# Optimization experiments

Measured on AMD Instinct MI355X. Metric: run time of the kernel, lower is better.

## Reference

```python
import jax, jax.numpy as jnp
import numpy as np

B, L, C, H, W = 4, 8, 32, 128, 256
M1, M2 = 32, 32  # spectral modes


def setup_inputs() -> dict:
    key = jax.random.key(0)
    k1, k2, k3, k4, k5, k6 = jax.random.split(key, 6)
    scale = 1.0 / (C * C)
    return {
        "x": jax.random.normal(k1, (B, L, C, H, W), dtype=jnp.float32),
        "k": jax.random.normal(k2, (C, H, W), dtype=jnp.float32),
        "w1r": scale * jax.random.normal(k3, (C, C, M1, M2), dtype=jnp.float32),
        "w1i": scale * jax.random.normal(k4, (C, C, M1, M2), dtype=jnp.float32),
        "w2r": scale * jax.random.normal(k5, (C, C, M1, M2), dtype=jnp.float32),
        "w2i": scale * jax.random.normal(k6, (C, C, M1, M2), dtype=jnp.float32),
    }


def reference(x, k, w1r, w1i, w2r, w2i):
    # x: [B, L, C, H, W] real; k: [C, H, W] conv kernel (broadcast over B*L).
    b, l, c, h, w = x.shape
    # --- FlashFFTConvInterface fallback path: circular conv via rfft2.
    # H, W are already 2/3/5-smooth (next_fast_len is identity -> no padding).
    u = x.reshape(b * l, c, h, w)
    u_f = jnp.fft.rfft2(u)                     # [B*L, C, H, W//2+1] complex
    k_f = jnp.fft.rfft2(k)                     # [C, H, W//2+1], broadcasts
    y = jnp.fft.irfft2(u_f * k_f, s=(h, w)).reshape(b, l, c, h, w)

    # --- SpectralConv2d: per-mode channel mixing in frequency domain.
    x_f = jnp.fft.rfft2(y)                     # [B, L, C, H, Wf] complex
    wf = x_f.shape[-1]
    w1 = (w1r + 1j * w1i).astype(x_f.dtype)
    w2 = (w2r + 1j * w2i).astype(x_f.dtype)
    m1 = min(h, M1)
    m2 = min(wf, M2)
    co = w1.shape[1]
    top = jnp.einsum('blcij,coij->bloij', x_f[:, :, :, :m1, :m2], w1[:, :, :m1, :m2])
    out_f = jnp.zeros((b, l, co, h, wf), dtype=x_f.dtype)
    out_f = out_f.at[:, :, :, :m1, :m2].set(top)
    if h > 1 and (h > M1 or wf > M2):
        bot = jnp.einsum('blcij,coij->bloij', x_f[:, :, :, h - m1:, :m2], w2[:, :, :m1, :m2])
        out_f = out_f.at[:, :, :, h - m1:, :m2].set(bot)
    return jnp.fft.irfft2(out_f, s=(h, w))    # [B, L, Co, H, W] real
```

## Files before the change

kernel.cpp:

```cpp
#include <hip/hip_runtime.h>
#include <math.h>

#define Hn 128
#define Wn 256
#define PLANE (Hn*Wn)

#define OFF_TQC 0u
#define OFF_TQS 2048u
#define OFF_TP  4096u
#define OFF_KM  16384u
#define OFF_XM  147456u
#define OFF_B   4341760u
#define OFF_RK  12730368u

__global__ __launch_bounds__(256) void build_tables(float* __restrict__ ws) {
  int tid = blockIdx.x * 256 + threadIdx.x;
  const double PI2 = 6.283185307179586476925286766559;
  if (tid < 512) {
    int j = tid >> 4, xi = tid & 15;
    float cc[4], ss[4];
#pragma unroll
    for (int m = 0; m < 4; m++) {
      int x = xi * 4 + m;
      double ang = PI2 * (double)((j * x) & 255) / 256.0;
      cc[m] = (float)cos(ang); ss[m] = (float)sin(ang);
    }
    ((float4*)(ws + OFF_TQC))[tid] = make_float4(cc[0], cc[1], cc[2], cc[3]);
    ((float4*)(ws + OFF_TQS))[tid] = make_float4(ss[0], ss[1], ss[2], ss[3]);
  }
  if (tid < 2048) {
    int p = tid >> 6, y2 = tid & 63;
    double a0 = PI2 * (double)((p * (2 * y2)) & 127) / 128.0;
    double a1 = PI2 * (double)((p * (2 * y2 + 1)) & 127) / 128.0;
    ((float4*)(ws + OFF_TP))[tid] =
        make_float4((float)cos(a0), (float)sin(a0), (float)cos(a1), (float)sin(a1));
  }
}

__global__ __launch_bounds__(256, 3) void fwd_rows(const float* __restrict__ src,
                                                   float2* __restrict__ R,
                                                   const float* __restrict__ ws) {
  int plane = blockIdx.x >> 2, chunk = blockIdx.x & 3;
  __shared__ __align__(16) float Sd[32 * 260];
  __shared__ float4 Tc[544], Ts[544];
  int t = threadIdx.x;
  const float4* src4 = (const float4*)src;
  size_t sb = (size_t)plane * 8192 + (size_t)chunk * 2048;
#pragma unroll
  for (int k = 0; k < 8; k++) {
    int idx = t + 256 * k;
    int row = idx >> 6, c4 = idx & 63;
    int sws = (row >> 1) & 15;
    *(float4*)&Sd[row * 260 + ((c4 ^ sws) << 2)] = src4[sb + idx];
  }
  const float4* gTc = (const float4*)(ws + OFF_TQC);
  const float4* gTs = (const float4*)(ws + OFF_TQS);
#pragma unroll
  for (int k = 0; k < 2; k++) {
    int idx = t + 256 * k;
    Tc[(idx >> 4) * 17 + (idx & 15)] = gTc[idx];
    Ts[(idx >> 4) * 17 + (idx & 15)] = gTs[idx];
  }
  __syncthreads();
  float eA[4][4], oA[4][4];
#pragma unroll
  for (int uu = 0; uu < 4; uu++) {
    int unit = uu * 256 + t;
    int y = unit >> 5, xb = unit & 31;
    int sws = (y >> 1) & 15;
    const float* rowp = &Sd[y * 260];
    float4 A = *(const float4*)&rowp[(xb ^ sws) << 2];
    float Av[4] = {A.x, A.y, A.z, A.w};
    float M[4];
#pragma unroll
    for (int kk = 0; kk < 4; kk++) {
      int xm = 256 - 4 * xb - kk;
      int xmc = (xm > 255) ? 255 : xm;
      int c4m = xmc >> 2, e = xmc & 3;
      float v = rowp[((c4m ^ sws) << 2) + e];
      M[kk] = (xm > 255) ? 0.f : v;
    }
#pragma unroll
    for (int kk = 0; kk < 4; kk++) {
      eA[uu][kk] = Av[kk] + M[kk];
      oA[uu][kk] = Av[kk] - M[kk];
    }
    if (xb == 0) {
      oA[uu][0] = rowp[(32 ^ sws) << 2];
    }
  }
  __syncthreads();
#pragma unroll
  for (int uu = 0; uu < 4; uu++) {
    int unit = uu * 256 + t;
    int y = unit >> 5, xb = unit & 31;
    int sws = (y >> 1) & 15;
    float* rowp = &Sd[y * 260];
    *(float4*)&rowp[(xb ^ sws) << 2] =
        make_float4(eA[uu][0], eA[uu][1], eA[uu][2], eA[uu][3]);
    *(float4*)&rowp[((32 + xb) ^ sws) << 2] =
        make_float4(oA[uu][0], oA[uu][1], oA[uu][2], oA[uu][3]);
  }
  __syncthreads();
  int jg = t & 15, yg = t >> 4;
  int jm = jg & 3;
  const float4* pC0 = &Tc[jg * 17];
  const float4* pS0 = &Ts[jg * 17];
  const float4* pC1 = &Tc[(jg + 16) * 17];
  const float4* pS1 = &Ts[(jg + 16) * 17];
  const float4* p2_0 = (jm & 1) ? pS0 : pC0;
  const float4* p4_0 = (jm & 1) ? pC0 : pS0;
  const float4* p2_1 = (jm & 1) ? pS1 : pC1;
  const float4* p4_1 = (jm & 1) ? pC1 : pS1;
  float sa = (jm == 0 || jm == 3) ? 1.f : -1.f;
  float sb_ = (jm < 2) ? 1.f : -1.f;
  float pm = (jg & 1) ? -1.f : 1.f;
  int sw = yg & 15;
  const float* row0 = &Sd[(2 * yg) * 260];
  const float* row1 = &Sd[(2 * yg + 1) * 260];
  float d1[2][2], d2[2][2], d3[2][2], d4[2][2];
#pragma unroll
  for (int a = 0; a < 2; a++)
#pragma unroll
    for (int b = 0; b < 2; b++) { d1[a][b] = 0.f; d2[a][b] = 0.f; d3[a][b] = 0.f; d4[a][b] = 0.f; }
#define DOT4(a, b) (a.x * b.x + a.y * b.y + a.z * b.z + a.w * b.w)
#pragma unroll 4
  for (int xb = 0; xb < 16; xb++) {
    int off = (xb ^ sw) << 2;
    float4 e0y0 = *(const float4*)&row0[off];
    float4 e1y0 = *(const float4*)&row0[off + 64];
    float4 o0y0 = *(const float4*)&row0[off + 128];
    float4 o1y0 = *(const float4*)&row0[off + 192];
    float4 e0y1 = *(const float4*)&row1[off];
    float4 e1y1 = *(const float4*)&row1[off + 64];
    float4 o0y1 = *(const float4*)&row1[off + 128];
    float4 o1y1 = *(const float4*)&row1[off + 192];
    float4 c0 = pC0[xb], s0 = pS0[xb];
    float4 t20 = p2_0[xb], t40 = p4_0[xb];
    float4 c1 = pC1[xb], s1 = pS1[xb];
    float4 t21 = p2_1[xb], t41 = p4_1[xb];
    d1[0][0] += DOT4(e0y0, c0);  d1[0][1] += DOT4(e0y1, c0);
    d1[1][0] += DOT4(e0y0, c1);  d1[1][1] += DOT4(e0y1, c1);
    d2[0][0] += DOT4(e1y0, t20); d2[0][1] += DOT4(e1y1, t20);
    d2[1][0] += DOT4(e1y0, t21); d2[1][1] += DOT4(e1y1, t21);
    d3[0][0] += DOT4(o0y0, s0);  d3[0][1] += DOT4(o0y1, s0);
    d3[1][0] += DOT4(o0y0, s1);  d3[1][1] += DOT4(o0y1, s1);
    d4[0][0] += DOT4(o1y0, t40); d4[0][1] += DOT4(o1y1, t40);
    d4[1][0] += DOT4(o1y0, t41); d4[1][1] += DOT4(o1y1, t41);
  }
#undef DOT4
  float u128_0 = row0[128 + 4 * sw];
  float u128_1 = row1[128 + 4 * sw];
#pragma unroll
  for (int jj = 0; jj < 2; jj++) {
    int j = jg + 16 * jj;
#pragma unroll
    for (int ky = 0; ky < 2; ky++) {
      int y = chunk * 32 + yg * 2 + ky;
      float u128 = ky ? u128_1 : u128_0;
      float re = d1[jj][ky] + sa * d2[jj][ky] + pm * u128;
      float im = -(d3[jj][ky] + sb_ * d4[jj][ky]);
      R[((size_t)plane * 128 + y) * 32 + j] = make_float2(re, im);
    }
  }
}

__global__ __launch_bounds__(256) void fwd_cols(const float2* __restrict__ Rg,
                                                float2* __restrict__ dst,
                                                const float* __restrict__ ws) {
  int plane = blockIdx.x;
  __shared__ float4 Rs4[2048];
  __shared__ float4 TPs[2048];
  float2* Rs = (float2*)Rs4;
  int t = threadIdx.x;
  const float4* in4 = (const float4*)(Rg + (size_t)plane * 4096);
#pragma unroll
  for (int k = 0; k < 8; k++) Rs4[t + 256 * k] = in4[t + 256 * k];
  const float4* gTP = (const float4*)(ws + OFF_TP);
#pragma unroll
  for (int k = 0; k < 8; k++) TPs[t + 256 * k] = gTP[t + 256 * k];
  __syncthreads();
  int j = t & 31, pg = t >> 5;
  float Are[4], Aim[4], Bre[4], Bim[4];
#pragma unroll
  for (int m = 0; m < 4; m++) { Are[m] = Aim[m] = Bre[m] = Bim[m] = 0.f; }
  for (int it = 0; it < 32; it++) {
#pragma unroll
    for (int h = 0; h < 2; h++) {
      int y2 = 2 * it + h;
      float sg = (h == 0) ? 1.f : -1.f;
      float2 r0 = Rs[(2 * y2) * 32 + j];
      float2 r1 = Rs[(2 * y2 + 1) * 32 + j];
#pragma unroll
      for (int m = 0; m < 4; m++) {
        int p = pg + 8 * m;
        float4 tw = TPs[p * 64 + y2];
        float P0 = r0.x * tw.x + r0.y * tw.y;
        float Q0 = r0.y * tw.x - r0.x * tw.y;
        float P1 = r1.x * tw.z + r1.y * tw.w;
        float Q1 = r1.y * tw.z - r1.x * tw.w;
        Are[m] += P0 + P1;
        Aim[m] += Q0 + Q1;
        Bre[m] += sg * (P0 - Q1);
        Bim[m] += sg * (Q0 + P1);
      }
    }
  }
  size_t ob = (size_t)plane * 2048;
#pragma unroll
  for (int m = 0; m < 4; m++) {
    int p = pg + 8 * m;
    dst[ob + p * 32 + j] = make_float2(Are[m], Aim[m]);
    dst[ob + (32 + p) * 32 + j] = make_float2(Bre[m], Bim[m]);
  }
}

__global__ __launch_bounds__(256) void wk_build(const float* __restrict__ w1r,
                                                const float* __restrict__ w1i,
                                                const float* __restrict__ w2r,
                                                const float* __restrict__ w2i,
                                                float2* __restrict__ wk,
                                                const float2* __restrict__ km) {
  int e0 = blockIdx.x * 256 + threadIdx.x;
#pragma unroll
  for (int k = 0; k < 4; k++) {
    int e = e0 + k * 524288;
    int o = e & 31, c = (e >> 5) & 31, j = (e >> 10) & 31, i64 = e >> 15;
    int r = (i64 < 32) ? i64 : i64 - 32;
    const float* wr = (i64 < 32) ? w1r : w2r;
    const float* wi = (i64 < 32) ? w1i : w2i;
    int widx = ((c * 32 + o) * 32 + r) * 32 + j;
    float wrv = wr[widx], wiv = wi[widx];
    float2 kv = km[(size_t)c * 2048 + i64 * 32 + j];
    wk[e] = make_float2(kv.x * wrv - kv.y * wiv, kv.x * wiv + kv.y * wrv);
  }
}

__global__ __launch_bounds__(256) void mix_modes(float2* __restrict__ xm,
                                                 const float2* __restrict__ wk) {
  int bid = blockIdx.x;
  int mode = (bid & 7) * 256 + (bid >> 3);
  __shared__ float4 Xs4[512], Ws4[512];
  float2* Xs = (float2*)Xs4;
  float2* Wsl = (float2*)Ws4;
  int t = threadIdx.x;
#pragma unroll
  for (int k = 0; k < 4; k++) {
    int p = t + 256 * k;
    Xs[p] = xm[(size_t)p * 2048 + mode];
  }
  const float4* wk4 = (const float4*)(wk + (size_t)mode * 1024);
#pragma unroll
  for (int k = 0; k < 2; k++) Ws4[t + 256 * k] = wk4[t + 256 * k];
  __syncthreads();
  int o = t & 31, bg = t >> 5;
  float orr[4], oii[4];
#pragma unroll
  for (int m = 0; m < 4; m++) { orr[m] = 0.f; oii[m] = 0.f; }
  for (int c2 = 0; c2 < 16; c2++) {
    float2 w0 = Wsl[(2 * c2) * 32 + o];
    float2 w1 = Wsl[(2 * c2 + 1) * 32 + o];
#pragma unroll
    for (int m = 0; m < 4; m++) {
      float4 xv = *(const float4*)&Xs[(bg * 4 + m) * 32 + 2 * c2];
      orr[m] += xv.x * w0.x - xv.y * w0.y + xv.z * w1.x - xv.w * w1.y;
      oii[m] += xv.x * w0.y + xv.y * w0.x + xv.z * w1.y + xv.w * w1.x;
    }
  }
#pragma unroll
  for (int m = 0; m < 4; m++)
    xm[(size_t)((bg * 4 + m) * 32 + o) * 2048 + mode] = make_float2(orr[m], oii[m]);
}

__global__ __launch_bounds__(256) void inv_rows(const float2* __restrict__ om,
                                                float2* __restrict__ G,
                                                const float* __restrict__ ws) {
  int plane = blockIdx.x;
  __shared__ float4 Os4[1024];
  __shared__ float4 TPs[2048];
  float2* Os = (float2*)Os4;
  int t = threadIdx.x;
  const float4* in4 = (const float4*)(om + (size_t)plane * 2048);
#pragma unroll
  for (int k = 0; k < 4; k++) Os4[t + 256 * k] = in4[t + 256 * k];
  const float4* gTP = (const float4*)(ws + OFF_TP);
#pragma unroll
  for (int k = 0; k < 8; k++) TPs[t + 256 * k] = gTP[t + 256 * k];
  __syncthreads();
  int j = t & 31, yg = t >> 5;
  float gr[16], gi[16];
#pragma unroll
  for (int k = 0; k < 16; k++) { gr[k] = 0.f; gi[k] = 0.f; }
  for (int p = 0; p < 32; p++) {
    float2 A = Os[p * 32 + j];
    float2 B = Os[(32 + p) * 32 + j];
#pragma unroll
    for (int mp = 0; mp < 8; mp++) {
      int y2 = yg * 8 + mp;
      float4 tw = TPs[p * 64 + y2];
      float sg = ((mp & 1) == 0) ? 1.f : -1.f;
      float Sr = A.x + sg * B.x, Si = A.y + sg * B.y;
      gr[2 * mp]     += Sr * tw.x - Si * tw.y;
      gi[2 * mp]     += Sr * tw.y + Si * tw.x;
      float Tr = A.x + sg * B.y, Ti = A.y - sg * B.x;
      gr[2 * mp + 1] += Tr * tw.z - Ti * tw.w;
      gi[2 * mp + 1] += Tr * tw.w + Ti * tw.z;
    }
  }
  const float inv = 1.0f / 32768.0f;
  size_t gb = (size_t)plane * 128;
#pragma unroll
  for (int mm = 0; mm < 16; mm++) {
    int y = yg * 16 + mm;
    float sr = (j == 0) ? gr[mm] * inv : 2.f * inv * gr[mm];
    float si = (j == 0) ? 0.f : 2.f * inv * gi[mm];
    G[(gb + y) * 32 + j] = make_float2(sr, si);
  }
}

__global__ __launch_bounds__(256) void inv_cols(const float2* __restrict__ G,
                                                float* __restrict__ out,
                                                const float* __restrict__ ws) {
  int plane = blockIdx.x >> 2, chunk = blockIdx.x & 3;
  __shared__ float2 Gs[32 * 33];
  __shared__ float4 Tc[544], Ts[544];
  int t = threadIdx.x;
  const float2* in = G + (size_t)plane * 4096 + (size_t)chunk * 1024;
#pragma unroll
  for (int k = 0; k < 4; k++) {
    int idx = t + 256 * k;
    Gs[(idx >> 5) * 33 + (idx & 31)] = in[idx];
  }
  const float4* gTc = (const float4*)(ws + OFF_TQC);
  const float4* gTs = (const float4*)(ws + OFF_TQS);
#pragma unroll
  for (int k = 0; k < 2; k++) {
    int idx = t + 256 * k;
    Tc[(idx >> 4) * 17 + (idx & 15)] = gTc[idx];
    Ts[(idx >> 4) * 17 + (idx & 15)] = gTs[idx];
  }
  __syncthreads();
  int xi = t & 15, yg = t >> 4;
  float4 acc[2][4];
#pragma unroll
  for (int ky = 0; ky < 2; ky++)
#pragma unroll
    for (int q = 0; q < 4; q++) acc[ky][q] = make_float4(0.f, 0.f, 0.f, 0.f);
  for (int jjb = 0; jjb < 8; jjb++) {
#pragma unroll
    for (int jjo = 0; jjo < 4; jjo++) {
      int jj = jjb * 4 + jjo;
      float4 c4 = Tc[jj * 17 + xi];
      float4 s4 = Ts[jj * 17 + xi];
#pragma unroll
      for (int ky = 0; ky < 2; ky++) {
        float2 g = Gs[(yg * 2 + ky) * 33 + jj];
        float4 P, Q;
        P.x = g.x * c4.x - g.y * s4.x;  P.y = g.x * c4.y - g.y * s4.y;
        P.z = g.x * c4.z - g.y * s4.z;  P.w = g.x * c4.w - g.y * s4.w;
        Q.x = g.x * s4.x + g.y * c4.x;  Q.y = g.x * s4.y + g.y * c4.y;
        Q.z = g.x * s4.z + g.y * c4.z;  Q.w = g.x * s4.w + g.y * c4.w;
#pragma unroll
        for (int q = 0; q < 4; q++) {
          int m = (jjo * q) & 3;
          if (m == 0) {
            acc[ky][q].x += P.x; acc[ky][q].y += P.y; acc[ky][q].z += P.z; acc[ky][q].w += P.w;
          } else if (m == 1) {
            acc[ky][q].x -= Q.x; acc[ky][q].y -= Q.y; acc[ky][q].z -= Q.z; acc[ky][q].w -= Q.w;
          } else if (m == 2) {
            acc[ky][q].x -= P.x; acc[ky][q].y -= P.y; acc[ky][q].z -= P.z; acc[ky][q].w -= P.w;
          } else {
            acc[ky][q].x += Q.x; acc[ky][q].y += Q.y; acc[ky][q].z += Q.z; acc[ky][q].w += Q.w;
          }
        }
      }
    }
  }
  float* outp = out + (size_t)plane * PLANE + (size_t)chunk * 32 * Wn;
#pragma unroll
  for (int ky = 0; ky < 2; ky++) {
    int y = yg * 2 + ky;
#pragma unroll
    for (int q = 0; q < 4; q++)
      *(float4*)(outp + y * Wn + q * 64 + xi * 4) = acc[ky][q];
  }
}

extern "C" void kernel_launch(void* const* d_in, const int* in_sizes, int n_in,
                              void* d_out, int out_size, void* d_ws, size_t ws_size,
                              hipStream_t stream) {
  (void)in_sizes; (void)n_in; (void)out_size; (void)ws_size;
  const float* x   = (const float*)d_in[0];
  const float* kk  = (const float*)d_in[1];
  const float* w1r = (const float*)d_in[2];
  const float* w1i = (const float*)d_in[3];
  const float* w2r = (const float*)d_in[4];
  const float* w2i = (const float*)d_in[5];
  float*  ws   = (float*)d_ws;
  float*  out  = (float*)d_out;
  float2* km2  = (float2*)(ws + OFF_KM);
  float2* xm2  = (float2*)(ws + OFF_XM);
  float2* bx   = (float2*)(ws + OFF_B);
  float2* rk   = (float2*)(ws + OFF_RK);

  build_tables<<<8, 256, 0, stream>>>(ws);
  fwd_rows<<<4096, 256, 0, stream>>>(x, bx, ws);
  fwd_rows<<<128, 256, 0, stream>>>(kk, rk, ws);
  fwd_cols<<<1024, 256, 0, stream>>>(bx, xm2, ws);
  fwd_cols<<<32, 256, 0, stream>>>(rk, km2, ws);
  wk_build<<<2048, 256, 0, stream>>>(w1r, w1i, w2r, w2i, bx, km2);
  mix_modes<<<2048, 256, 0, stream>>>(xm2, bx);
  inv_rows<<<1024, 256, 0, stream>>>(xm2, bx, ws);
  inv_cols<<<4096, 256, 0, stream>>>(bx, out, ws);
}
```

Before: 426.4 us.

## Exploit real-output symmetry in final inverse DFT to halve table work

Rewrites the final real-output inverse DFT stage so each thread accumulates even and odd frequency contributions against cosine and sine tables separately. Outputs for x, 128±x and 256−x are then reconstructed from the symmetric and antisymmetric combinations, with the x=64 and x=192 columns handled by special scalar sums. This cuts the complex multiply-add work and the quadrant sign-switch logic of the previous accumulation. In exchange, the tail writes become scattered scalar stores rather than float4 stores, and the index bookkeeping for the mirrored columns is more intricate.

```diff
diff --git a/kernel.cpp b/kernel.cpp
--- a/kernel.cpp
+++ b/kernel.cpp
@@ -341,48 +341,67 @@
   }
   __syncthreads();
   int xi = t & 15, yg = t >> 4;
-  float4 acc[2][4];
-#pragma unroll
-  for (int ky = 0; ky < 2; ky++)
-#pragma unroll
-    for (int q = 0; q < 4; q++) acc[ky][q] = make_float4(0.f, 0.f, 0.f, 0.f);
-  for (int jjb = 0; jjb < 8; jjb++) {
-#pragma unroll
-    for (int jjo = 0; jjo < 4; jjo++) {
-      int jj = jjb * 4 + jjo;
-      float4 c4 = Tc[jj * 17 + xi];
-      float4 s4 = Ts[jj * 17 + xi];
-#pragma unroll
-      for (int ky = 0; ky < 2; ky++) {
-        float2 g = Gs[(yg * 2 + ky) * 33 + jj];
-        float4 P, Q;
-        P.x = g.x * c4.x - g.y * s4.x;  P.y = g.x * c4.y - g.y * s4.y;
-        P.z = g.x * c4.z - g.y * s4.z;  P.w = g.x * c4.w - g.y * s4.w;
-        Q.x = g.x * s4.x + g.y * c4.x;  Q.y = g.x * s4.y + g.y * c4.y;
-        Q.z = g.x * s4.z + g.y * c4.z;  Q.w = g.x * s4.w + g.y * c4.w;
-#pragma unroll
-        for (int q = 0; q < 4; q++) {
-          int m = (jjo * q) & 3;
-          if (m == 0) {
-            acc[ky][q].x += P.x; acc[ky][q].y += P.y; acc[ky][q].z += P.z; acc[ky][q].w += P.w;
-          } else if (m == 1) {
-            acc[ky][q].x -= Q.x; acc[ky][q].y -= Q.y; acc[ky][q].z -= Q.z; acc[ky][q].w -= Q.w;
-          } else if (m == 2) {
-            acc[ky][q].x -= P.x; acc[ky][q].y -= P.y; acc[ky][q].z -= P.z; acc[ky][q].w -= P.w;
-          } else {
-            acc[ky][q].x += Q.x; acc[ky][q].y += Q.y; acc[ky][q].z += Q.z; acc[ky][q].w += Q.w;
-          }
-        }
-      }
-    }
-  }
+  float4 Ce[2], Co[2], Se[2], So[2];
+  float c64[2], s64[2];
+#pragma unroll
+  for (int ky = 0; ky < 2; ky++) {
+    Ce[ky] = make_float4(0.f, 0.f, 0.f, 0.f);
+    Co[ky] = make_float4(0.f, 0.f, 0.f, 0.f);
+    Se[ky] = make_float4(0.f, 0.f, 0.f, 0.f);
+    So[ky] = make_float4(0.f, 0.f, 0.f, 0.f);
+    c64[ky] = 0.f; s64[ky] = 0.f;
+  }
+#define FMA4(acc, s, v) do { acc.x += (s) * (v).x; acc.y += (s) * (v).y; \
+                             acc.z += (s) * (v).z; acc.w += (s) * (v).w; } while (0)
+#pragma unroll 4
+  for (int jh = 0; jh < 16; jh++) {
+    float4 ce = Tc[(2 * jh) * 17 + xi],     se = Ts[(2 * jh) * 17 + xi];
+    float4 co = Tc[(2 * jh + 1) * 17 + xi], so = Ts[(2 * jh + 1) * 17 + xi];
+    float sgn = (jh & 1) ? -1.f : 1.f;
+#pragma unroll
+    for (int ky = 0; ky < 2; ky++) {
+      float2 ge = Gs[(yg * 2 + ky) * 33 + 2 * jh];
+      float2 go = Gs[(yg * 2 + ky) * 33 + 2 * jh + 1];
+      FMA4(Ce[ky], ge.x, ce);
+      FMA4(Se[ky], ge.y, se);
+      FMA4(Co[ky], go.x, co);
+      FMA4(So[ky], go.y, so);
+      c64[ky] += sgn * ge.x;
+      s64[ky] += sgn * go.y;
+    }
+  }
+#undef FMA4
   float* outp = out + (size_t)plane * PLANE + (size_t)chunk * 32 * Wn;
 #pragma unroll
   for (int ky = 0; ky < 2; ky++) {
     int y = yg * 2 + ky;
-#pragma unroll
-    for (int q = 0; q < 4; q++)
-      *(float4*)(outp + y * Wn + q * 64 + xi * 4) = acc[ky][q];
+    float* ro = outp + y * Wn;
+    float4 C  = make_float4(Ce[ky].x + Co[ky].x, Ce[ky].y + Co[ky].y,
+                            Ce[ky].z + Co[ky].z, Ce[ky].w + Co[ky].w);
+    float4 Cm = make_float4(Ce[ky].x - Co[ky].x, Ce[ky].y - Co[ky].y,
+                            Ce[ky].z - Co[ky].z, Ce[ky].w - Co[ky].w);
+    float4 S  = make_float4(Se[ky].x + So[ky].x, Se[ky].y + So[ky].y,
+                            Se[ky].z + So[ky].z, Se[ky].w + So[ky].w);
+    float4 Sm = make_float4(So[ky].x - Se[ky].x, So[ky].y - Se[ky].y,
+                            So[ky].z - Se[ky].z, So[ky].w - Se[ky].w);
+    *(float4*)(ro + 4 * xi) =
+        make_float4(C.x - S.x, C.y - S.y, C.z - S.z, C.w - S.w);
+    *(float4*)(ro + 128 + 4 * xi) =
+        make_float4(Cm.x + Sm.x, Cm.y + Sm.y, Cm.z + Sm.z, Cm.w + Sm.w);
+    int mb = 128 - 4 * xi;
+    ro[mb]     = Cm.x - Sm.x;
+    ro[mb - 1] = Cm.y - Sm.y;
+    ro[mb - 2] = Cm.z - Sm.z;
+    ro[mb - 3] = Cm.w - Sm.w;
+    int nb = 256 - 4 * xi;
+    if (xi) ro[nb] = C.x + S.x;
+    ro[nb - 1] = C.y + S.y;
+    ro[nb - 2] = C.z + S.z;
+    ro[nb - 3] = C.w + S.w;
+    if (xi == 0) {
+      ro[64]  = c64[ky] - s64[ky];
+      ro[192] = c64[ky] + s64[ky];
+    }
   }
 }
 
```

After: 425.3 us. No clear change (-0.3%).
